# Kernel optimization log

Hardware: AMD Instinct MI355X
Metric: run time of the kernel (lower is better)

## Reference

```python
import jax, jax.numpy as jnp
import numpy as np

B, S, E, H = 2, 2048, 1024, 16
D = E // H  # head dim = 64

def setup_inputs() -> dict:
    key = jax.random.key(0)
    ks = jax.random.split(key, 7)
    mk = lambda k, shape, scale=1.0: (jax.random.normal(k, shape, dtype=jnp.float32) * scale)
    return {
        "query": mk(ks[0], (B, S, E)),
        "key": mk(ks[1], (B, S, E)),
        "value": mk(ks[2], (B, S, E)),
        "Wq": mk(ks[3], (E, E), 1.0 / np.sqrt(E)),
        "Wk": mk(ks[4], (E, E), 1.0 / np.sqrt(E)),
        "Wv": mk(ks[5], (E, E), 1.0 / np.sqrt(E)),
        "Wo": mk(ks[6], (E, E), 1.0 / np.sqrt(E)),
    }

def reference(query, key, value, Wq, Wk, Wv, Wo):
    # nn.Linear(bias=False): y = x @ W.T
    def split_heads(x):
        return x.reshape(B, -1, H, D).transpose(0, 2, 1, 3)  # [B,H,S,D]
    q = split_heads(query @ Wq.T)
    k = split_heads(key @ Wk.T)
    v = split_heads(value @ Wv.T)
    scores = jnp.einsum("bhqd,bhkd->bhqk", q, k) / jnp.sqrt(jnp.float32(D))
    attn = jax.nn.softmax(scores, axis=-1)  # dropout p=0 -> identity
    out = jnp.einsum("bhqk,bhkd->bhqd", attn, v)
    out = out.transpose(0, 2, 1, 3).reshape(B, -1, E)
    out = out @ Wo.T
    return out
```

## Files before the change

### kernel.cpp

```cpp
#include <hip/hip_runtime.h>
#include <stdint.h>

#define S_LEN 2048
#define HDIM  64
#define EMB   1024
#define NTOK  4096

typedef short bf16x8 __attribute__((ext_vector_type(8)));
typedef float f32x4  __attribute__((ext_vector_type(4)));
typedef uint32_t u32x4 __attribute__((ext_vector_type(4)));
typedef uint32_t u32x2 __attribute__((ext_vector_type(2)));

__device__ __forceinline__ unsigned short f32_bf16(float f) {
  union { float f; uint32_t u; } v; v.f = f;
  return (unsigned short)((v.u + 0x7fffu + ((v.u >> 16) & 1u)) >> 16);
}

__device__ __forceinline__ uint32_t fbits(float f) {
  union { float f; uint32_t u; } v; v.f = f; return v.u;
}

__device__ __forceinline__ uint32_t pack_bf16_trunc(float lo, float hi) {
  return __builtin_amdgcn_perm(fbits(hi), fbits(lo), 0x07060302u);
}

__device__ __forceinline__ uint32_t pack_bf16_rne(float lo, float hi) {
  return (uint32_t)f32_bf16(lo) | ((uint32_t)f32_bf16(hi) << 16);
}

__device__ __forceinline__ void async_ld16(const unsigned short* g, unsigned short* l) {
  __builtin_amdgcn_global_load_lds(
      (__attribute__((address_space(1))) unsigned int*)(uintptr_t)g,
      (__attribute__((address_space(3))) unsigned int*)l, 16, 0, 0);
}

__device__ __forceinline__ void p_swap(uint32_t& x, uint32_t& y) {
  u32x2 r1 = __builtin_amdgcn_permlane32_swap(x, y, false, false);
  uint32_t a = r1[0], b = r1[1];
#if __has_builtin(__builtin_amdgcn_permlane16_swap)
  u32x2 r2 = __builtin_amdgcn_permlane16_swap(a, b, false, false);
  x = r2[0]; y = r2[1];
#else
  asm volatile("v_permlane16_swap_b32 %0, %1" : "+v"(a), "+v"(b));
  x = a; y = b;
#endif
}

__device__ __forceinline__ void block_sync_lgkm() {
  asm volatile("s_waitcnt lgkmcnt(0)" ::: "memory");
  __builtin_amdgcn_s_barrier();
}

#define CL2 0.18033688f

__global__ void cast_all(const float* __restrict__ q, const float* __restrict__ k,
                         const float* __restrict__ v, const float* __restrict__ Wq,
                         const float* __restrict__ Wk, const float* __restrict__ Wv,
                         const float* __restrict__ Wo,
                         unsigned short* __restrict__ qb, unsigned short* __restrict__ kb,
                         unsigned short* __restrict__ vb, unsigned short* __restrict__ wqb,
                         unsigned short* __restrict__ wkb, unsigned short* __restrict__ wvb,
                         unsigned short* __restrict__ wob) {
  const int b = blockIdx.x;
  const float* src; unsigned short* dst; int base;
  float scl = 1.0f;
  if (b < 12288) {
    const int which = b >> 12; base = b & 4095;
    src = which == 0 ? q : which == 1 ? k : v;
    dst = which == 0 ? qb : which == 1 ? kb : vb;
  } else {
    const int bb = b - 12288, which = bb >> 10; base = bb & 1023;
    src = which == 0 ? Wq : which == 1 ? Wk : which == 2 ? Wv : Wo;
    dst = which == 0 ? wqb : which == 1 ? wkb : which == 2 ? wvb : wob;
    if (which == 0) scl = CL2;
  }
  const int i = base * 256 + threadIdx.x;
  float4 f = ((const float4*)src)[i];
  ushort4 o;
  o.x = f32_bf16(f.x * scl); o.y = f32_bf16(f.y * scl);
  o.z = f32_bf16(f.z * scl); o.w = f32_bf16(f.w * scl);
  ((ushort4*)dst)[i] = o;
}

__global__ __launch_bounds__(256)
void gemm_qkv(const unsigned short* __restrict__ qb, const unsigned short* __restrict__ kb,
              const unsigned short* __restrict__ vb, const unsigned short* __restrict__ wqb,
              const unsigned short* __restrict__ wkb, const unsigned short* __restrict__ wvb,
              unsigned short* __restrict__ Qh, unsigned short* __restrict__ Kh,
              unsigned short* __restrict__ Vt) {
  __shared__ __align__(16) unsigned short As[2 * 128 * 32];
  __shared__ __align__(16) unsigned short Bs[2 * 128 * 32];

  const int z  = blockIdx.z;
  const int bx = blockIdx.y;
  const int by = blockIdx.x;
  const unsigned short* Xp = z == 0 ? qb  : z == 1 ? kb  : vb;
  const unsigned short* Wp = z == 0 ? wqb : z == 1 ? wkb : wvb;

  const unsigned short *A, *B;
  int tileM, tileN;
  if (z < 2) { A = Wp; tileM = bx * 128; B = Xp; tileN = by * 128; }
  else       { A = Xp; tileM = by * 128; B = Wp; tileN = bx * 128; }

  const int tid  = threadIdx.x;
  const int lane = tid & 63;
  const int wave = tid >> 6;
  const int wm = (wave >> 1) * 64;
  const int wn = (wave & 1) * 64;
  const int ccol = lane & 15;
  const int cgrp = lane >> 4;
  const int rchunk = lane >> 2;
  const int coff   = (lane & 3) * 8;

  f32x4 acc[4][4];
#pragma unroll
  for (int i = 0; i < 4; ++i)
#pragma unroll
    for (int j = 0; j < 4; ++j) acc[i][j] = 0.f;

  for (int k0 = 0; k0 < EMB; k0 += 64) {
#pragma unroll
    for (int kk = 0; kk < 2; ++kk)
#pragma unroll
      for (int i = 0; i < 2; ++i) {
        const int c = wave * 2 + i;
        const int row = c * 16 + rchunk;
        async_ld16(A + (size_t)(tileM + row) * EMB + k0 + kk * 32 + coff,
                   As + kk * 4096 + c * 512);
        async_ld16(B + (size_t)(tileN + row) * EMB + k0 + kk * 32 + coff,
                   Bs + kk * 4096 + c * 512);
      }
    __syncthreads();
#pragma unroll
    for (int kk = 0; kk < 2; ++kk) {
      bf16x8 af[4], bfm[4];
#pragma unroll
      for (int i = 0; i < 4; ++i) {
        af[i]  = *(const bf16x8*)(As + kk * 4096 + (wm + i * 16 + ccol) * 32 + cgrp * 8);
        bfm[i] = *(const bf16x8*)(Bs + kk * 4096 + (wn + i * 16 + ccol) * 32 + cgrp * 8);
      }
#pragma unroll
      for (int i = 0; i < 4; ++i)
#pragma unroll
        for (int j = 0; j < 4; ++j)
          acc[i][j] = __builtin_amdgcn_mfma_f32_16x16x32_bf16(af[i], bfm[j], acc[i][j], 0, 0, 0);
    }
    __syncthreads();
  }

  if (z < 2) {
    unsigned short* Oh = (z == 0) ? Qh : Kh;
#pragma unroll
    for (int i = 0; i < 4; ++i) {
      const int gd = tileM + wm + i * 16 + cgrp * 4;
      const int h = gd >> 6, dd = gd & 63;
#pragma unroll
      for (int j = 0; j < 4; ++j) {
        const int gt = tileN + wn + j * 16 + ccol;
        const int b = gt >> 11, s = gt & 2047;
        const uint32_t u0 = pack_bf16_rne(acc[i][j][0], acc[i][j][1]);
        const uint32_t u1 = pack_bf16_rne(acc[i][j][2], acc[i][j][3]);
        *(int2*)&Oh[((size_t)((b * 16 + h) * 2048 + s)) * 64 + dd] =
            make_int2((int)u0, (int)u1);
      }
    }
  } else {
#pragma unroll
    for (int i = 0; i < 4; ++i) {
      const int gt = tileM + wm + i * 16 + cgrp * 4;
      const int b = gt >> 11, s = gt & 2047;
#pragma unroll
      for (int j = 0; j < 4; ++j) {
        const int gd = tileN + wn + j * 16 + ccol;
        const int h = gd >> 6, dd = gd & 63;
        const uint32_t u0 = pack_bf16_rne(acc[i][j][0], acc[i][j][1]);
        const uint32_t u1 = pack_bf16_rne(acc[i][j][2], acc[i][j][3]);
        *(int2*)&Vt[((size_t)((b * 16 + h) * 64 + dd)) * 2048 + s] =
            make_int2((int)u0, (int)u1);
      }
    }
  }
}

__global__ __launch_bounds__(256)
void gemm_out(const unsigned short* __restrict__ Ctx, const unsigned short* __restrict__ Wo,
              float* __restrict__ Out) {
  __shared__ __align__(16) unsigned short As[2 * 64 * 32];
  __shared__ __align__(16) unsigned short Bs[2 * 128 * 32];

  const int tid  = threadIdx.x;
  const int lane = tid & 63;
  const int wave = tid >> 6;
  const int wm = (wave >> 1) * 32;
  const int wn = (wave & 1) * 64;
  const int ccol = lane & 15;
  const int cgrp = lane >> 4;
  const int rchunk = lane >> 2;
  const int coff   = (lane & 3) * 8;
  const int tileM = blockIdx.y * 64;
  const int tileN = blockIdx.x * 128;

  f32x4 acc[2][4];
#pragma unroll
  for (int i = 0; i < 2; ++i)
#pragma unroll
    for (int j = 0; j < 4; ++j) acc[i][j] = 0.f;

  for (int k0 = 0; k0 < EMB; k0 += 64) {
#pragma unroll
    for (int kk = 0; kk < 2; ++kk) {
      {
        const int row = wave * 16 + rchunk;
        async_ld16(Wo + (size_t)(tileM + row) * EMB + k0 + kk * 32 + coff,
                   As + kk * 2048 + wave * 512);
      }
#pragma unroll
      for (int i = 0; i < 2; ++i) {
        const int c = wave * 2 + i;
        const int row = c * 16 + rchunk;
        async_ld16(Ctx + (size_t)(tileN + row) * EMB + k0 + kk * 32 + coff,
                   Bs + kk * 4096 + c * 512);
      }
    }
    __syncthreads();
#pragma unroll
    for (int kk = 0; kk < 2; ++kk) {
      bf16x8 af[2], bfm[4];
#pragma unroll
      for (int i = 0; i < 2; ++i)
        af[i] = *(const bf16x8*)(As + kk * 2048 + (wm + i * 16 + ccol) * 32 + cgrp * 8);
#pragma unroll
      for (int j = 0; j < 4; ++j)
        bfm[j] = *(const bf16x8*)(Bs + kk * 4096 + (wn + j * 16 + ccol) * 32 + cgrp * 8);
#pragma unroll
      for (int i = 0; i < 2; ++i)
#pragma unroll
        for (int j = 0; j < 4; ++j)
          acc[i][j] = __builtin_amdgcn_mfma_f32_16x16x32_bf16(af[i], bfm[j], acc[i][j], 0, 0, 0);
    }
    __syncthreads();
  }

#pragma unroll
  for (int i = 0; i < 2; ++i) {
    const int odim = tileM + wm + i * 16 + cgrp * 4;
#pragma unroll
    for (int j = 0; j < 4; ++j) {
      const int gt = tileN + wn + j * 16 + ccol;
      float4 o = make_float4(acc[i][j][0], acc[i][j][1], acc[i][j][2], acc[i][j][3]);
      *(float4*)&Out[(size_t)gt * 1024 + odim] = o;
    }
  }
}

__global__ __launch_bounds__(256, 2)
void attn_kernel(const unsigned short* __restrict__ Qh,
                 const unsigned short* __restrict__ Kh,
                 const unsigned short* __restrict__ Vt,
                 unsigned short* __restrict__ Ctx) {
  __shared__ __align__(16) unsigned short Ks[2 * 64 * 64];
  __shared__ __align__(16) unsigned short Vs[2 * 64 * 64];
  __shared__ __align__(16) unsigned short Ps[128 * 64];

  const int tid  = threadIdx.x;
  const int lane = tid & 63;
  const int wave = tid >> 6;
  const int bh = blockIdx.x;
  const int q0 = blockIdx.y * 128;
  const unsigned short* Qg = Qh + ((size_t)bh * S_LEN + q0) * HDIM;
  const unsigned short* Kg = Kh + (size_t)bh * S_LEN * HDIM;
  const unsigned short* Vg = Vt + (size_t)bh * HDIM * S_LEN;

  const int ccol = lane & 15;
  const int cgrp = lane >> 4;
  const int mrow = wave * 32;
  const int sw7  = ccol & 7;

#pragma unroll
  for (int i = 0; i < 4; ++i) {
    const int cid = i * 256 + tid;
    const int row = cid >> 3, j = cid & 7, g = j ^ (row & 7);
    *(int4*)&Ps[row * 64 + j * 8] = *(const int4*)&Qg[(size_t)row * 64 + g * 8];
  }

  const int r0 = tid >> 3, j0 = tid & 7;
  const int r1 = r0 + 32;
  const int sA = j0 ^ (r0 & 7);
  const int sB = j0 ^ (r1 & 7);

  int4 kr0 = *(const int4*)&Kg[(size_t)r0 * 64 + sA * 8];
  int4 kr1 = *(const int4*)&Kg[(size_t)r1 * 64 + sB * 8];
  int4 vr0 = *(const int4*)&Vg[(size_t)r0 * 2048 + sA * 8];
  int4 vr1 = *(const int4*)&Vg[(size_t)r1 * 2048 + sB * 8];

  __syncthreads();

  bf16x8 aq[2][2];
#pragma unroll
  for (int g = 0; g < 2; ++g)
#pragma unroll
    for (int kk = 0; kk < 2; ++kk) {
      const int pp = (kk * 4 + cgrp) ^ sw7;
      aq[g][kk] = *(const bf16x8*)&Ps[(mrow + g * 16 + ccol) * 64 + pp * 8];
    }

  *(int4*)&Ks[r0 * 64 + j0 * 8] = kr0;
  *(int4*)&Ks[r1 * 64 + j0 * 8] = kr1;
  *(int4*)&Vs[r0 * 64 + j0 * 8] = vr0;
  *(int4*)&Vs[r1 * 64 + j0 * 8] = vr1;
  kr0 = *(const int4*)&Kg[(size_t)(64 + r0) * 64 + sA * 8];
  kr1 = *(const int4*)&Kg[(size_t)(64 + r1) * 64 + sB * 8];
  vr0 = *(const int4*)&Vg[(size_t)r0 * 2048 + 64 + sA * 8];
  vr1 = *(const int4*)&Vg[(size_t)r1 * 2048 + 64 + sB * 8];
  block_sync_lgkm();

  f32x4 l4[2];
  l4[0] = 0.f; l4[1] = 0.f;
  f32x4 o_acc[4][2];
#pragma unroll
  for (int dt = 0; dt < 4; ++dt) { o_acc[dt][0] = 0.f; o_acc[dt][1] = 0.f; }

  for (int i = 0; i < 32; ++i) {
    unsigned short* Kb = Ks + (i & 1) * 4096;
    unsigned short* Vb = Vs + (i & 1) * 4096;

    f32x4 sc[2][4];
    __builtin_amdgcn_s_setprio(1);
#pragma unroll
    for (int nt = 0; nt < 4; ++nt) {
      const int krow = nt * 16 + ccol;
      bf16x8 ak0 = *(const bf16x8*)&Kb[krow * 64 + ((cgrp) ^ sw7) * 8];
      bf16x8 ak1 = *(const bf16x8*)&Kb[krow * 64 + ((4 + cgrp) ^ sw7) * 8];
#pragma unroll
      for (int g = 0; g < 2; ++g) {
        f32x4 s = 0.f;
        s = __builtin_amdgcn_mfma_f32_16x16x32_bf16(ak0, aq[g][0], s, 0, 0, 0);
        s = __builtin_amdgcn_mfma_f32_16x16x32_bf16(ak1, aq[g][1], s, 0, 0, 0);
        sc[g][nt] = s;
      }
    }
    __builtin_amdgcn_s_setprio(0);

    if (i < 31) {
      unsigned short* Kn = Ks + ((i + 1) & 1) * 4096;
      unsigned short* Vn = Vs + ((i + 1) & 1) * 4096;
      *(int4*)&Kn[r0 * 64 + j0 * 8] = kr0;
      *(int4*)&Kn[r1 * 64 + j0 * 8] = kr1;
      *(int4*)&Vn[r0 * 64 + j0 * 8] = vr0;
      *(int4*)&Vn[r1 * 64 + j0 * 8] = vr1;
      if (i < 30) {
        const int nb = (i + 2) * 64;
        kr0 = *(const int4*)&Kg[(size_t)(nb + r0) * 64 + sA * 8];
        kr1 = *(const int4*)&Kg[(size_t)(nb + r1) * 64 + sB * 8];
        vr0 = *(const int4*)&Vg[(size_t)r0 * 2048 + nb + sA * 8];
        vr1 = *(const int4*)&Vg[(size_t)r1 * 2048 + nb + sB * 8];
      }
    }

#pragma unroll
    for (int g = 0; g < 2; ++g)
#pragma unroll
      for (int nt = 0; nt < 4; ++nt) {
#pragma unroll
        for (int r = 0; r < 4; ++r)
          sc[g][nt][r] = __builtin_amdgcn_exp2f(sc[g][nt][r]);
        l4[g] += sc[g][nt];
      }

    bf16x8 ap[2][2];
#pragma unroll
    for (int g = 0; g < 2; ++g) {
      uint32_t u[4][2];
#pragma unroll
      for (int nt = 0; nt < 4; ++nt) {
        u[nt][0] = pack_bf16_trunc(sc[g][nt][0], sc[g][nt][1]);
        u[nt][1] = pack_bf16_trunc(sc[g][nt][2], sc[g][nt][3]);
      }
      uint32_t w[2][4];
#pragma unroll
      for (int kk = 0; kk < 2; ++kk)
#pragma unroll
        for (int h = 0; h < 2; ++h) {
          uint32_t x = u[2 * kk][h], y = u[2 * kk + 1][h];
          p_swap(x, y);
          w[kk][h] = x; w[kk][2 + h] = y;
        }
#pragma unroll
      for (int kk = 0; kk < 2; ++kk) {
        union { u32x4 u; bf16x8 b; } cv;
        cv.u[0] = w[kk][0]; cv.u[1] = w[kk][1];
        cv.u[2] = w[kk][2]; cv.u[3] = w[kk][3];
        ap[g][kk] = cv.b;
      }
    }

    __builtin_amdgcn_s_setprio(1);
#pragma unroll
    for (int dt = 0; dt < 4; ++dt) {
      const int vrow = dt * 16 + ccol;
      bf16x8 av0 = *(const bf16x8*)&Vb[vrow * 64 + ((cgrp) ^ sw7) * 8];
      bf16x8 av1 = *(const bf16x8*)&Vb[vrow * 64 + ((4 + cgrp) ^ sw7) * 8];
#pragma unroll
      for (int g = 0; g < 2; ++g) {
        f32x4 o = o_acc[dt][g];
        o = __builtin_amdgcn_mfma_f32_16x16x32_bf16(av0, ap[g][0], o, 0, 0, 0);
        o = __builtin_amdgcn_mfma_f32_16x16x32_bf16(av1, ap[g][1], o, 0, 0, 0);
        o_acc[dt][g] = o;
      }
    }
    __builtin_amdgcn_s_setprio(0);

    block_sync_lgkm();
  }

  const int b = bh >> 4, h = bh & 15;
#pragma unroll
  for (int g = 0; g < 2; ++g) {
    float l_i = l4[g][0] + l4[g][1] + l4[g][2] + l4[g][3];
    l_i += __shfl_xor(l_i, 16);
    l_i += __shfl_xor(l_i, 32);
    const float inv_l = __builtin_amdgcn_rcpf(l_i) * 1.00195f;
    const int srow = q0 + mrow + g * 16 + ccol;
#pragma unroll
    for (int dt = 0; dt < 4; ++dt) {
      float o0 = o_acc[dt][g][0] * inv_l, o1 = o_acc[dt][g][1] * inv_l;
      float o2 = o_acc[dt][g][2] * inv_l, o3 = o_acc[dt][g][3] * inv_l;
      uint32_t u0 = pack_bf16_rne(o0, o1);
      uint32_t u1 = pack_bf16_rne(o2, o3);
      const int col = h * 64 + dt * 16 + cgrp * 4;
      *(int2*)&Ctx[((size_t)(b * 2048 + srow)) * 1024 + col] = make_int2((int)u0, (int)u1);
    }
  }
}

extern "C" void kernel_launch(void* const* d_in, const int* in_sizes, int n_in,
                              void* d_out, int out_size, void* d_ws, size_t ws_size,
                              hipStream_t stream) {
  const float* q  = (const float*)d_in[0];
  const float* k  = (const float*)d_in[1];
  const float* v  = (const float*)d_in[2];
  const float* Wq = (const float*)d_in[3];
  const float* Wk = (const float*)d_in[4];
  const float* Wv = (const float*)d_in[5];
  const float* Wo = (const float*)d_in[6];

  const size_t tok = (size_t)NTOK * EMB;
  const size_t wsz = (size_t)EMB * EMB;
  unsigned short* p = (unsigned short*)d_ws;
  unsigned short* qb  = p; p += tok;
  unsigned short* kb  = p; p += tok;
  unsigned short* vb  = p; p += tok;
  unsigned short* wqb = p; p += wsz;
  unsigned short* wkb = p; p += wsz;
  unsigned short* wvb = p; p += wsz;
  unsigned short* wob = p; p += wsz;
  unsigned short* Qh  = p; p += tok;
  unsigned short* Kh  = p; p += tok;
  unsigned short* Vt  = p; p += tok;
  unsigned short* Ctx = p; p += tok;

  cast_all<<<dim3(16384), dim3(256), 0, stream>>>(q, k, v, Wq, Wk, Wv, Wo,
                                                  qb, kb, vb, wqb, wkb, wvb, wob);

  gemm_qkv<<<dim3(32, 8, 3), dim3(256), 0, stream>>>(qb, kb, vb, wqb, wkb, wvb,
                                                     Qh, Kh, Vt);

  attn_kernel<<<dim3(32, 16), dim3(256), 0, stream>>>(Qh, Kh, Vt, Ctx);

  gemm_out<<<dim3(32, 16), dim3(256), 0, stream>>>(Ctx, wob, (float*)d_out);
}
```

Measured before the change: 205.8 us.

## Halve attention query tile to 64 rows with two-wave blocks

The attention kernel now runs 128-thread blocks that each own 64 query rows, doubling the grid to 32x32 blocks. The separate Q staging buffer is dropped and Q is staged through the K buffer instead, which cuts shared memory per block. The aim is more resident blocks per CU and better load balance across the GPU. The cost is that each K/V tile is fetched from global memory twice as often overall, and each thread now issues more loads per tile.

```diff
diff --git a/kernel.cpp b/kernel.cpp
--- a/kernel.cpp
+++ b/kernel.cpp
@@ -253,20 +253,19 @@
   }
 }
 
-__global__ __launch_bounds__(256, 2)
+__global__ __launch_bounds__(128, 2)
 void attn_kernel(const unsigned short* __restrict__ Qh,
                  const unsigned short* __restrict__ Kh,
                  const unsigned short* __restrict__ Vt,
                  unsigned short* __restrict__ Ctx) {
   __shared__ __align__(16) unsigned short Ks[2 * 64 * 64];
   __shared__ __align__(16) unsigned short Vs[2 * 64 * 64];
-  __shared__ __align__(16) unsigned short Ps[128 * 64];
 
   const int tid  = threadIdx.x;
   const int lane = tid & 63;
   const int wave = tid >> 6;
   const int bh = blockIdx.x;
-  const int q0 = blockIdx.y * 128;
+  const int q0 = blockIdx.y * 64;
   const unsigned short* Qg = Qh + ((size_t)bh * S_LEN + q0) * HDIM;
   const unsigned short* Kg = Kh + (size_t)bh * S_LEN * HDIM;
   const unsigned short* Vg = Vt + (size_t)bh * HDIM * S_LEN;
@@ -278,40 +277,42 @@
 
 #pragma unroll
   for (int i = 0; i < 4; ++i) {
-    const int cid = i * 256 + tid;
+    const int cid = i * 128 + tid;
     const int row = cid >> 3, j = cid & 7, g = j ^ (row & 7);
-    *(int4*)&Ps[row * 64 + j * 8] = *(const int4*)&Qg[(size_t)row * 64 + g * 8];
-  }
-
-  const int r0 = tid >> 3, j0 = tid & 7;
-  const int r1 = r0 + 32;
-  const int sA = j0 ^ (r0 & 7);
-  const int sB = j0 ^ (r1 & 7);
-
-  int4 kr0 = *(const int4*)&Kg[(size_t)r0 * 64 + sA * 8];
-  int4 kr1 = *(const int4*)&Kg[(size_t)r1 * 64 + sB * 8];
-  int4 vr0 = *(const int4*)&Vg[(size_t)r0 * 2048 + sA * 8];
-  int4 vr1 = *(const int4*)&Vg[(size_t)r1 * 2048 + sB * 8];
-
+    *(int4*)&Ks[row * 64 + j * 8] = *(const int4*)&Qg[(size_t)row * 64 + g * 8];
+  }
   __syncthreads();
-
   bf16x8 aq[2][2];
 #pragma unroll
   for (int g = 0; g < 2; ++g)
 #pragma unroll
     for (int kk = 0; kk < 2; ++kk) {
       const int pp = (kk * 4 + cgrp) ^ sw7;
-      aq[g][kk] = *(const bf16x8*)&Ps[(mrow + g * 16 + ccol) * 64 + pp * 8];
-    }
-
-  *(int4*)&Ks[r0 * 64 + j0 * 8] = kr0;
-  *(int4*)&Ks[r1 * 64 + j0 * 8] = kr1;
-  *(int4*)&Vs[r0 * 64 + j0 * 8] = vr0;
-  *(int4*)&Vs[r1 * 64 + j0 * 8] = vr1;
-  kr0 = *(const int4*)&Kg[(size_t)(64 + r0) * 64 + sA * 8];
-  kr1 = *(const int4*)&Kg[(size_t)(64 + r1) * 64 + sB * 8];
-  vr0 = *(const int4*)&Vg[(size_t)r0 * 2048 + 64 + sA * 8];
-  vr1 = *(const int4*)&Vg[(size_t)r1 * 2048 + 64 + sB * 8];
+      aq[g][kk] = *(const bf16x8*)&Ks[(mrow + g * 16 + ccol) * 64 + pp * 8];
+    }
+  block_sync_lgkm();
+
+  const int r0 = tid >> 3, j0 = tid & 7;
+  const int sA = j0 ^ (r0 & 7);
+  int4 kr[4], vr[4];
+#pragma unroll
+  for (int c = 0; c < 4; ++c) {
+    const int r = r0 + 16 * c;
+    kr[c] = *(const int4*)&Kg[(size_t)r * 64 + sA * 8];
+    vr[c] = *(const int4*)&Vg[(size_t)r * 2048 + sA * 8];
+  }
+#pragma unroll
+  for (int c = 0; c < 4; ++c) {
+    const int r = r0 + 16 * c;
+    *(int4*)&Ks[r * 64 + j0 * 8] = kr[c];
+    *(int4*)&Vs[r * 64 + j0 * 8] = vr[c];
+  }
+#pragma unroll
+  for (int c = 0; c < 4; ++c) {
+    const int r = r0 + 16 * c;
+    kr[c] = *(const int4*)&Kg[(size_t)(64 + r) * 64 + sA * 8];
+    vr[c] = *(const int4*)&Vg[(size_t)r * 2048 + 64 + sA * 8];
+  }
   block_sync_lgkm();
 
   f32x4 l4[2];
@@ -344,16 +345,20 @@
     if (i < 31) {
       unsigned short* Kn = Ks + ((i + 1) & 1) * 4096;
       unsigned short* Vn = Vs + ((i + 1) & 1) * 4096;
-      *(int4*)&Kn[r0 * 64 + j0 * 8] = kr0;
-      *(int4*)&Kn[r1 * 64 + j0 * 8] = kr1;
-      *(int4*)&Vn[r0 * 64 + j0 * 8] = vr0;
-      *(int4*)&Vn[r1 * 64 + j0 * 8] = vr1;
+#pragma unroll
+      for (int c = 0; c < 4; ++c) {
+        const int r = r0 + 16 * c;
+        *(int4*)&Kn[r * 64 + j0 * 8] = kr[c];
+        *(int4*)&Vn[r * 64 + j0 * 8] = vr[c];
+      }
       if (i < 30) {
         const int nb = (i + 2) * 64;
-        kr0 = *(const int4*)&Kg[(size_t)(nb + r0) * 64 + sA * 8];
-        kr1 = *(const int4*)&Kg[(size_t)(nb + r1) * 64 + sB * 8];
-        vr0 = *(const int4*)&Vg[(size_t)r0 * 2048 + nb + sA * 8];
-        vr1 = *(const int4*)&Vg[(size_t)r1 * 2048 + nb + sB * 8];
+#pragma unroll
+        for (int c = 0; c < 4; ++c) {
+          const int r = r0 + 16 * c;
+          kr[c] = *(const int4*)&Kg[(size_t)(nb + r) * 64 + sA * 8];
+          vr[c] = *(const int4*)&Vg[(size_t)r * 2048 + nb + sA * 8];
+        }
       }
     }
 
@@ -465,7 +470,7 @@
   gemm_qkv<<<dim3(32, 8, 3), dim3(256), 0, stream>>>(qb, kb, vb, wqb, wkb, wvb,
                                                      Qh, Kh, Vt);
 
-  attn_kernel<<<dim3(32, 16), dim3(256), 0, stream>>>(Qh, Kh, Vt, Ctx);
+  attn_kernel<<<dim3(32, 32), dim3(128), 0, stream>>>(Qh, Kh, Vt, Ctx);
 
   gemm_out<<<dim3(32, 16), dim3(256), 0, stream>>>(Ctx, wob, (float*)d_out);
 }
```

New measurement: 320.1 us. +55.6%, slower.

## Double-buffer LDS tiles in projection GEMMs to overlap loads with MFMA

Applied to the files above, without the earlier changes.

Both the QKV projection and output projection GEMMs now prefetch the next 32-wide K slice into an alternate LDS buffer while computing on the current one. This replaces the load-then-sync-then-compute pattern with one sync per step. It halves the K step per iteration, doubling loop trips and barriers, and relies on async loads completing by the end-of-iteration barrier.

```diff
diff --git a/kernel.cpp b/kernel.cpp
--- a/kernel.cpp
+++ b/kernel.cpp
@@ -118,33 +118,38 @@
 #pragma unroll
     for (int j = 0; j < 4; ++j) acc[i][j] = 0.f;
 
-  for (int k0 = 0; k0 < EMB; k0 += 64) {
-#pragma unroll
-    for (int kk = 0; kk < 2; ++kk)
+#pragma unroll
+  for (int i = 0; i < 2; ++i) {
+    const int c = wave * 2 + i;
+    const int row = c * 16 + rchunk;
+    async_ld16(A + (size_t)(tileM + row) * EMB + coff, As + c * 512);
+    async_ld16(B + (size_t)(tileN + row) * EMB + coff, Bs + c * 512);
+  }
+  __syncthreads();
+
+  for (int s = 0; s < 32; ++s) {
+    const int p = s & 1;
+    if (s < 31) {
+      const int kb0 = (s + 1) * 32, q = p ^ 1;
 #pragma unroll
       for (int i = 0; i < 2; ++i) {
         const int c = wave * 2 + i;
         const int row = c * 16 + rchunk;
-        async_ld16(A + (size_t)(tileM + row) * EMB + k0 + kk * 32 + coff,
-                   As + kk * 4096 + c * 512);
-        async_ld16(B + (size_t)(tileN + row) * EMB + k0 + kk * 32 + coff,
-                   Bs + kk * 4096 + c * 512);
-      }
-    __syncthreads();
-#pragma unroll
-    for (int kk = 0; kk < 2; ++kk) {
-      bf16x8 af[4], bfm[4];
-#pragma unroll
-      for (int i = 0; i < 4; ++i) {
-        af[i]  = *(const bf16x8*)(As + kk * 4096 + (wm + i * 16 + ccol) * 32 + cgrp * 8);
-        bfm[i] = *(const bf16x8*)(Bs + kk * 4096 + (wn + i * 16 + ccol) * 32 + cgrp * 8);
-      }
-#pragma unroll
-      for (int i = 0; i < 4; ++i)
-#pragma unroll
-        for (int j = 0; j < 4; ++j)
-          acc[i][j] = __builtin_amdgcn_mfma_f32_16x16x32_bf16(af[i], bfm[j], acc[i][j], 0, 0, 0);
-    }
+        async_ld16(A + (size_t)(tileM + row) * EMB + kb0 + coff, As + q * 4096 + c * 512);
+        async_ld16(B + (size_t)(tileN + row) * EMB + kb0 + coff, Bs + q * 4096 + c * 512);
+      }
+    }
+    bf16x8 af[4], bfm[4];
+#pragma unroll
+    for (int i = 0; i < 4; ++i) {
+      af[i]  = *(const bf16x8*)(As + p * 4096 + (wm + i * 16 + ccol) * 32 + cgrp * 8);
+      bfm[i] = *(const bf16x8*)(Bs + p * 4096 + (wn + i * 16 + ccol) * 32 + cgrp * 8);
+    }
+#pragma unroll
+    for (int i = 0; i < 4; ++i)
+#pragma unroll
+      for (int j = 0; j < 4; ++j)
+        acc[i][j] = __builtin_amdgcn_mfma_f32_16x16x32_bf16(af[i], bfm[j], acc[i][j], 0, 0, 0);
     __syncthreads();
   }
 
@@ -206,38 +211,45 @@
 #pragma unroll
     for (int j = 0; j < 4; ++j) acc[i][j] = 0.f;
 
-  for (int k0 = 0; k0 < EMB; k0 += 64) {
-#pragma unroll
-    for (int kk = 0; kk < 2; ++kk) {
+  {
+    const int row = wave * 16 + rchunk;
+    async_ld16(Wo + (size_t)(tileM + row) * EMB + coff, As + wave * 512);
+  }
+#pragma unroll
+  for (int i = 0; i < 2; ++i) {
+    const int c = wave * 2 + i;
+    const int row = c * 16 + rchunk;
+    async_ld16(Ctx + (size_t)(tileN + row) * EMB + coff, Bs + c * 512);
+  }
+  __syncthreads();
+
+  for (int s = 0; s < 32; ++s) {
+    const int p = s & 1;
+    if (s < 31) {
+      const int kb0 = (s + 1) * 32, q = p ^ 1;
       {
         const int row = wave * 16 + rchunk;
-        async_ld16(Wo + (size_t)(tileM + row) * EMB + k0 + kk * 32 + coff,
-                   As + kk * 2048 + wave * 512);
+        async_ld16(Wo + (size_t)(tileM + row) * EMB + kb0 + coff, As + q * 2048 + wave * 512);
       }
 #pragma unroll
       for (int i = 0; i < 2; ++i) {
         const int c = wave * 2 + i;
         const int row = c * 16 + rchunk;
-        async_ld16(Ctx + (size_t)(tileN + row) * EMB + k0 + kk * 32 + coff,
-                   Bs + kk * 4096 + c * 512);
-      }
-    }
-    __syncthreads();
-#pragma unroll
-    for (int kk = 0; kk < 2; ++kk) {
-      bf16x8 af[2], bfm[4];
-#pragma unroll
-      for (int i = 0; i < 2; ++i)
-        af[i] = *(const bf16x8*)(As + kk * 2048 + (wm + i * 16 + ccol) * 32 + cgrp * 8);
+        async_ld16(Ctx + (size_t)(tileN + row) * EMB + kb0 + coff, Bs + q * 4096 + c * 512);
+      }
+    }
+    bf16x8 af[2], bfm[4];
+#pragma unroll
+    for (int i = 0; i < 2; ++i)
+      af[i] = *(const bf16x8*)(As + p * 2048 + (wm + i * 16 + ccol) * 32 + cgrp * 8);
+#pragma unroll
+    for (int j = 0; j < 4; ++j)
+      bfm[j] = *(const bf16x8*)(Bs + p * 4096 + (wn + j * 16 + ccol) * 32 + cgrp * 8);
+#pragma unroll
+    for (int i = 0; i < 2; ++i)
 #pragma unroll
       for (int j = 0; j < 4; ++j)
-        bfm[j] = *(const bf16x8*)(Bs + kk * 4096 + (wn + j * 16 + ccol) * 32 + cgrp * 8);
-#pragma unroll
-      for (int i = 0; i < 2; ++i)
-#pragma unroll
-        for (int j = 0; j < 4; ++j)
-          acc[i][j] = __builtin_amdgcn_mfma_f32_16x16x32_bf16(af[i], bfm[j], acc[i][j], 0, 0, 0);
-    }
+        acc[i][j] = __builtin_amdgcn_mfma_f32_16x16x32_bf16(af[i], bfm[j], acc[i][j], 0, 0, 0);
     __syncthreads();
   }
 
```

Result: slower. 213.2 us (+3.6%).

## Split attention over two key halves and merge partials in a combine kernel

Applied to the files above, without the earlier changes.

The attention kernel now launches a third grid dimension that splits the 2048 keys into two halves. Each half writes unnormalized fp32 partial outputs and row sums to scratch buffers reused from d_out and dead input buffers. A new combine kernel adds the partials, normalizes and converts to bf16. The Q staging buffer is folded into the K LDS buffer, and launch bounds are raised to allow more resident blocks, so the two changes together aim for more parallelism and occupancy. The cost is 16MB-scale fp32 partial writes and reads plus an extra kernel launch.

```diff
diff --git a/kernel.cpp b/kernel.cpp
--- a/kernel.cpp
+++ b/kernel.cpp
@@ -253,23 +253,24 @@
   }
 }
 
-__global__ __launch_bounds__(256, 2)
+__global__ __launch_bounds__(256, 4)
 void attn_kernel(const unsigned short* __restrict__ Qh,
                  const unsigned short* __restrict__ Kh,
                  const unsigned short* __restrict__ Vt,
-                 unsigned short* __restrict__ Ctx) {
+                 float* __restrict__ Po0, float* __restrict__ Po1,
+                 float* __restrict__ lbuf) {
   __shared__ __align__(16) unsigned short Ks[2 * 64 * 64];
   __shared__ __align__(16) unsigned short Vs[2 * 64 * 64];
-  __shared__ __align__(16) unsigned short Ps[128 * 64];
 
   const int tid  = threadIdx.x;
   const int lane = tid & 63;
   const int wave = tid >> 6;
   const int bh = blockIdx.x;
   const int q0 = blockIdx.y * 128;
+  const int z  = blockIdx.z;
   const unsigned short* Qg = Qh + ((size_t)bh * S_LEN + q0) * HDIM;
-  const unsigned short* Kg = Kh + (size_t)bh * S_LEN * HDIM;
-  const unsigned short* Vg = Vt + (size_t)bh * HDIM * S_LEN;
+  const unsigned short* Kg = Kh + (size_t)bh * S_LEN * HDIM + (size_t)z * 1024 * HDIM;
+  const unsigned short* Vg = Vt + (size_t)bh * HDIM * S_LEN + (size_t)z * 1024;
 
   const int ccol = lane & 15;
   const int cgrp = lane >> 4;
@@ -280,7 +281,7 @@
   for (int i = 0; i < 4; ++i) {
     const int cid = i * 256 + tid;
     const int row = cid >> 3, j = cid & 7, g = j ^ (row & 7);
-    *(int4*)&Ps[row * 64 + j * 8] = *(const int4*)&Qg[(size_t)row * 64 + g * 8];
+    *(int4*)&Ks[row * 64 + j * 8] = *(const int4*)&Qg[(size_t)row * 64 + g * 8];
   }
 
   const int r0 = tid >> 3, j0 = tid & 7;
@@ -301,8 +302,9 @@
 #pragma unroll
     for (int kk = 0; kk < 2; ++kk) {
       const int pp = (kk * 4 + cgrp) ^ sw7;
-      aq[g][kk] = *(const bf16x8*)&Ps[(mrow + g * 16 + ccol) * 64 + pp * 8];
-    }
+      aq[g][kk] = *(const bf16x8*)&Ks[(mrow + g * 16 + ccol) * 64 + pp * 8];
+    }
+  block_sync_lgkm();
 
   *(int4*)&Ks[r0 * 64 + j0 * 8] = kr0;
   *(int4*)&Ks[r1 * 64 + j0 * 8] = kr1;
@@ -320,7 +322,7 @@
 #pragma unroll
   for (int dt = 0; dt < 4; ++dt) { o_acc[dt][0] = 0.f; o_acc[dt][1] = 0.f; }
 
-  for (int i = 0; i < 32; ++i) {
+  for (int i = 0; i < 16; ++i) {
     unsigned short* Kb = Ks + (i & 1) * 4096;
     unsigned short* Vb = Vs + (i & 1) * 4096;
 
@@ -341,14 +343,14 @@
     }
     __builtin_amdgcn_s_setprio(0);
 
-    if (i < 31) {
+    if (i < 15) {
       unsigned short* Kn = Ks + ((i + 1) & 1) * 4096;
       unsigned short* Vn = Vs + ((i + 1) & 1) * 4096;
       *(int4*)&Kn[r0 * 64 + j0 * 8] = kr0;
       *(int4*)&Kn[r1 * 64 + j0 * 8] = kr1;
       *(int4*)&Vn[r0 * 64 + j0 * 8] = vr0;
       *(int4*)&Vn[r1 * 64 + j0 * 8] = vr1;
-      if (i < 30) {
+      if (i < 14) {
         const int nb = (i + 2) * 64;
         kr0 = *(const int4*)&Kg[(size_t)(nb + r0) * 64 + sA * 8];
         kr1 = *(const int4*)&Kg[(size_t)(nb + r1) * 64 + sB * 8];
@@ -414,23 +416,41 @@
   }
 
   const int b = bh >> 4, h = bh & 15;
+  float* Po = z ? Po1 : Po0;
 #pragma unroll
   for (int g = 0; g < 2; ++g) {
     float l_i = l4[g][0] + l4[g][1] + l4[g][2] + l4[g][3];
     l_i += __shfl_xor(l_i, 16);
     l_i += __shfl_xor(l_i, 32);
-    const float inv_l = __builtin_amdgcn_rcpf(l_i) * 1.00195f;
     const int srow = q0 + mrow + g * 16 + ccol;
+    if (cgrp == 0)
+      lbuf[(size_t)z * 65536 + bh * 2048 + srow] = l_i;
 #pragma unroll
     for (int dt = 0; dt < 4; ++dt) {
-      float o0 = o_acc[dt][g][0] * inv_l, o1 = o_acc[dt][g][1] * inv_l;
-      float o2 = o_acc[dt][g][2] * inv_l, o3 = o_acc[dt][g][3] * inv_l;
-      uint32_t u0 = pack_bf16_rne(o0, o1);
-      uint32_t u1 = pack_bf16_rne(o2, o3);
       const int col = h * 64 + dt * 16 + cgrp * 4;
-      *(int2*)&Ctx[((size_t)(b * 2048 + srow)) * 1024 + col] = make_int2((int)u0, (int)u1);
-    }
-  }
+      *(f32x4*)&Po[((size_t)(b * 2048 + srow)) * 1024 + col] = o_acc[dt][g];
+    }
+  }
+}
+
+__global__ __launch_bounds__(256)
+void combine_attn(const float* __restrict__ Po0, const float* __restrict__ Po1,
+                  const float* __restrict__ lbuf, unsigned short* __restrict__ Ctx) {
+  const int idx = blockIdx.x * 256 + threadIdx.x;
+  const size_t e0 = (size_t)idx * 4;
+  const int row = (int)(e0 >> 10);
+  const int col = (int)(e0 & 1023);
+  const int h = col >> 6;
+  const int b = row >> 11, srow = row & 2047;
+  const int lrow = (b * 16 + h) * 2048 + srow;
+  const float la = lbuf[lrow];
+  const float lb2 = lbuf[65536 + lrow];
+  const float inv = __builtin_amdgcn_rcpf(la + lb2) * 1.00195f;
+  f32x4 a = *(const f32x4*)&Po0[e0];
+  f32x4 c = *(const f32x4*)&Po1[e0];
+  const uint32_t u0 = pack_bf16_rne((a[0] + c[0]) * inv, (a[1] + c[1]) * inv);
+  const uint32_t u1 = pack_bf16_rne((a[2] + c[2]) * inv, (a[3] + c[3]) * inv);
+  *(int2*)&Ctx[e0] = make_int2((int)u0, (int)u1);
 }
 
 extern "C" void kernel_launch(void* const* d_in, const int* in_sizes, int n_in,
@@ -459,13 +479,19 @@
   unsigned short* Vt  = p; p += tok;
   unsigned short* Ctx = p; p += tok;
 
+  float* Po0  = (float*)d_out;
+  float* Po1  = (float*)qb;
+  float* lbuf = (float*)vb;
+
   cast_all<<<dim3(16384), dim3(256), 0, stream>>>(q, k, v, Wq, Wk, Wv, Wo,
                                                   qb, kb, vb, wqb, wkb, wvb, wob);
 
   gemm_qkv<<<dim3(32, 8, 3), dim3(256), 0, stream>>>(qb, kb, vb, wqb, wkb, wvb,
                                                      Qh, Kh, Vt);
 
-  attn_kernel<<<dim3(32, 16), dim3(256), 0, stream>>>(Qh, Kh, Vt, Ctx);
+  attn_kernel<<<dim3(32, 16, 2), dim3(256), 0, stream>>>(Qh, Kh, Vt, Po0, Po1, lbuf);
+
+  combine_attn<<<dim3(4096), dim3(256), 0, stream>>>(Po0, Po1, lbuf, Ctx);
 
   gemm_out<<<dim3(32, 16), dim3(256), 0, stream>>>(Ctx, wob, (float*)d_out);
 }
```

After: 215.7 us. 4.8% more time.
